# Kernel optimization log

Hardware: AMD Instinct MI355X
Metric: run time of the kernel (lower is better)

The kernel has to match this reference:

```python
import jax, jax.numpy as jnp
import numpy as np

# ---- static module configuration ----
N_POU = 16
N_BC = 3
P = N_POU + N_BC          # full_n_pou = 19
F = 3                      # n_fields
B, N, D_IN, D_Z, D_H = 16, 1024, 32, 64, 64
N_DIR = 64
MAX_ITERS = 50
ALPHA = 0.1                # damped fixed-point step of the nonlinear solver

# edge_pairs / delta_0 for the complete graph on P POU nodes (construct_delta0)
_ei, _ej = np.triu_indices(P, 1)
E = _ei.shape[0]           # n_one_forms = P*(P-1)/2 = 171
_d0 = np.zeros((E, P), np.float32)
_d0[np.arange(E), _ei] = -1.0
_d0[np.arange(E), _ej] = 1.0
DELTA0 = jnp.asarray(_d0)  # [E, P]
EI = jnp.asarray(_ei)
EJ = jnp.asarray(_ej)


def setup_inputs() -> dict:
    key = jax.random.key(0)
    ks = jax.random.split(key, 16)
    f32 = jnp.float32
    inp = {
        'in_tokens': jax.random.normal(ks[0], (B, N, D_IN), f32),
        'K_list': 0.02 * jax.random.normal(ks[1], (B, F, N, N), f32),
        'M_list': 0.02 * jax.random.normal(ks[2], (B, F, N, N), f32),
        'dirichlet_nodes': jax.random.randint(ks[3], (B, N_DIR), 0, N),
        'boundary_vals': jax.random.normal(ks[4], (B, N_DIR, F), f32),
        'u_init': jax.random.normal(ks[5], (B, P * F), f32),
        # learned parameters (encoder / source_model / boundary_w / flux_model)
        'W_enc': jax.random.normal(ks[6], (D_IN, D_Z), f32) / np.sqrt(D_IN),
        'b_enc': jnp.zeros((D_Z,), f32),
        'W_src': jax.random.normal(ks[7], (D_Z, F), f32) / np.sqrt(D_Z),
        'b_src': jnp.zeros((F,), f32),
        'W_pou': jax.random.normal(ks[8], (D_Z, P * F), f32) / np.sqrt(D_Z),
        'Wf1': jax.random.normal(ks[9], (2 * F, D_H), f32) / np.sqrt(2 * F),
        'Wz': jax.random.normal(ks[10], (D_Z, D_H), f32) / np.sqrt(D_Z),
        'bf': jnp.zeros((D_H,), f32),
        'Wf2': 0.1 * jax.random.normal(ks[11], (D_H, F), f32) / np.sqrt(D_H),
    }
    return inp


def reference(in_tokens, K_list, M_list, dirichlet_nodes, boundary_vals, u_init,
              W_enc, b_enc, W_src, b_src, W_pou, Wf1, Wz, bf, Wf2):
    Bc, Nn = in_tokens.shape[0], in_tokens.shape[1]
    latent_scaling = Nn / P

    # encoder: in_tokens -> per-node latents z [B,N,Dz]
    z = jnp.tanh(in_tokens @ W_enc + b_enc)

    # boundary_w: partition-of-unity weights W [B,P,N,F], boundary POUs biased
    # toward Dirichlet nodes via boundary_vals
    logits = (z @ W_pou).reshape(Bc, Nn, P, F)
    bidx = jnp.arange(Bc)[:, None]
    bvals_full = jnp.zeros((Bc, Nn, F), in_tokens.dtype).at[bidx, dirichlet_nodes].set(boundary_vals)
    logits = logits.at[:, :, P - N_BC:, :].add(bvals_full[:, :, None, :])
    Wmat = jax.nn.softmax(logits, axis=2).transpose(0, 2, 1, 3)  # [B,P,N,F]

    # source_model + latent projection (source_mode='identity' -> pass-through)
    f_full = z @ W_src + b_src                                    # [B,N,F]
    f_latent = jnp.einsum('bpif,bif->bpf', Wmat, f_full) / latent_scaling

    # project_bilinear_per_field: K_hat[b,p,q,f] = W K W^T / scaling
    def project(Kl):
        t = jnp.einsum('bpif,bfij->bpjf', Wmat, Kl)               # [B,P,N,F]
        return jnp.einsum('bpjf,bqjf->bpqf', t, Wmat) / latent_scaling

    # apply_dirichlet_per_field: boundary rows -> identity
    eyeP = jnp.eye(P, dtype=in_tokens.dtype)
    row_mask = jnp.zeros((P,), bool).at[P - N_BC:].set(True)
    def dirichlet_bilinear(Kh):
        return jnp.where(row_mask[None, :, None, None], eyeP[None, :, :, None], Kh)

    K_hat = dirichlet_bilinear(project(K_list))                   # [B,P,P,F]
    M_hat = dirichlet_bilinear(project(M_list))

    bc_mask = jnp.zeros((P, F), bool).at[P - N_BC:, :].set(True)
    bc_vals = jnp.zeros((P, F), in_tokens.dtype).at[P - N_BC, :].set(1.0)

    # flux_model conditioning: pooled latent, precomputed once
    zp = jnp.mean(z, axis=1) @ Wz                                 # [B,Dh]
    src_term = jnp.einsum('bpqf,bqf->bpf', M_hat, f_latent)       # constant in u

    def G(u_flat):  # G_residual
        u = u_flat.reshape(Bc, P, F)
        diff_term = jnp.einsum('bpqf,bqf->bpf', K_hat, u)
        ue = jnp.concatenate([u[:, EI], u[:, EJ]], axis=-1)       # [B,E,2F]
        flux = jnp.tanh(ue @ Wf1 + zp[:, None, :] + bf) @ Wf2     # [B,E,F]
        flux_term = jnp.einsum('ep,bef->bpf', DELTA0, flux)
        r = diff_term - src_term - flux_term
        r = jnp.where(bc_mask[None], u - bc_vals[None], r)        # Dirichlet residual
        return r.reshape(Bc, -1)

    # NonlinearSolver: damped fixed-point iteration, fixed MAX_ITERS under jit
    def step(u, _):
        return u - ALPHA * G(u), None
    u_hat, _ = jax.lax.scan(step, u_init, None, length=MAX_ITERS)

    u_coarse = u_hat.reshape(Bc, P, F)
    u_fine = jnp.einsum('bpif,bpf->bif', Wmat, u_coarse)          # [B,N,F]
    return u_fine
```

## Files before the change

kernel.cpp:

```cpp
#include <hip/hip_runtime.h>

#define Bn 16
#define Nn 1024
#define DIN 32
#define DZ 64
#define Fc 3
#define Pp 19
#define PPAD 20
#define Ee 171
#define ITERS 50
#define INV_SCALE (19.0f/1024.0f)
#define CHUNK 64
#define PF 4

#define OFF_WPROJ 0
#define OFF_FFULL 983040
#define OFF_FLAT  1033216
#define OFF_UBUF  1034128
#define OFF_BVALS 1035040
#define OFF_ZACC  1084192
#define OFF_KHAT  1085216
#define OFF_SRC   1099808
#define ZERO_FLOATS 65536

__global__ __launch_bounds__(1024) void k_scatter(const int* __restrict__ nodes,
                                                  const float* __restrict__ bvals,
                                                  float* __restrict__ bfull) {
  __shared__ int sn[1024];
  int tid = threadIdx.x;
  sn[tid] = nodes[tid];
  __syncthreads();
  int b = tid >> 6, j = tid & 63;
  int node = sn[tid];
  bool win = true;
  for (int j2 = j + 1; j2 < 64; j2++)
    if (sn[(b << 6) | j2] == node) { win = false; break; }
  if (win) {
    #pragma unroll
    for (int f = 0; f < Fc; f++)
      bfull[((size_t)b*Nn + node)*Fc + f] = bvals[(size_t)tid*Fc + f];
  }
}

__global__ __launch_bounds__(128) void k_encode(
    const float* __restrict__ x, const float* __restrict__ Wenc, const float* __restrict__ benc,
    const float* __restrict__ Wsrc, const float* __restrict__ bsrc, const float* __restrict__ Wpou,
    const float* __restrict__ bfull, float* __restrict__ wproj, float* __restrict__ ffull,
    float* __restrict__ zacc) {
  __shared__ float sWenc[DIN*DZ];
  __shared__ float sWpou[DZ*57];
  __shared__ float sWsrc[DZ*Fc];
  int tid = threadIdx.x;
  for (int t = tid; t < DIN*DZ; t += 128) sWenc[t] = Wenc[t];
  for (int t = tid; t < DZ*57; t += 128) sWpou[t] = Wpou[t];
  for (int t = tid; t < DZ*Fc; t += 128) sWsrc[t] = Wsrc[t];
  __syncthreads();
  int g = blockIdx.x*128 + tid;
  int b = g >> 10, i = g & 1023;
  float xr[DIN];
  const float* xp = x + (size_t)g*DIN;
  #pragma unroll
  for (int k = 0; k < DIN; k += 4) {
    float4 t4 = *(const float4*)(xp + k);
    xr[k] = t4.x; xr[k+1] = t4.y; xr[k+2] = t4.z; xr[k+3] = t4.w;
  }
  float l[57];
  #pragma unroll
  for (int o = 0; o < 57; o++) l[o] = 0.f;
  float ff[3] = {bsrc[0], bsrc[1], bsrc[2]};
  int lane = tid & 63;
  for (int d = 0; d < DZ; d++) {
    float zd = benc[d];
    #pragma unroll
    for (int k = 0; k < DIN; k++) zd = fmaf(xr[k], sWenc[k*DZ + d], zd);
    zd = tanhf(zd);
    #pragma unroll
    for (int o = 0; o < 57; o++) l[o] = fmaf(zd, sWpou[d*57 + o], l[o]);
    #pragma unroll
    for (int f = 0; f < Fc; f++) ff[f] = fmaf(zd, sWsrc[d*Fc + f], ff[f]);
    float zs = zd;
    #pragma unroll
    for (int off = 32; off > 0; off >>= 1) zs += __shfl_xor(zs, off, 64);
    if (lane == 0) atomicAdd(&zacc[b*DZ + d], zs);
  }
  #pragma unroll
  for (int f = 0; f < Fc; f++) ffull[(size_t)g*Fc + f] = ff[f];
  #pragma unroll
  for (int f = 0; f < Fc; f++) {
    float bv = bfull[(size_t)g*Fc + f];
    l[16*3+f] += bv; l[17*3+f] += bv; l[18*3+f] += bv;
  }
  #pragma unroll
  for (int f = 0; f < Fc; f++) {
    float m = l[f];
    #pragma unroll
    for (int p = 1; p < Pp; p++) m = fmaxf(m, l[p*3+f]);
    float ex[Pp]; float s = 0.f;
    #pragma unroll
    for (int p = 0; p < Pp; p++) { ex[p] = __expf(l[p*3+f] - m); s += ex[p]; }
    float inv = 1.f / s;
    float* wp = wproj + ((size_t)(b*Fc + f)*Nn + i)*PPAD;
    #pragma unroll
    for (int p = 0; p < Pp; p++) wp[p] = ex[p]*inv;
  }
}

__global__ __launch_bounds__(256) void k_flat(const float* __restrict__ wproj,
                                              const float* __restrict__ ffull,
                                              float* __restrict__ flat) {
  int bf = blockIdx.x;
  int b = bf / 3, f = bf % 3;
  float acc[Pp];
  #pragma unroll
  for (int q = 0; q < Pp; q++) acc[q] = 0.f;
  for (int i = threadIdx.x; i < Nn; i += 256) {
    float fv = ffull[((size_t)b*Nn + i)*Fc + f];
    const float* row = wproj + ((size_t)bf*Nn + i)*PPAD;
    #pragma unroll
    for (int q = 0; q < Pp; q++) acc[q] = fmaf(row[q], fv, acc[q]);
  }
  #pragma unroll
  for (int q = 0; q < Pp; q++) {
    float v = acc[q];
    #pragma unroll
    for (int off = 32; off > 0; off >>= 1) v += __shfl_xor(v, off, 64);
    acc[q] = v;
  }
  __shared__ float red[4][Pp];
  int wave = threadIdx.x >> 6, lane = threadIdx.x & 63;
  if (lane == 0) {
    #pragma unroll
    for (int q = 0; q < Pp; q++) red[wave][q] = acc[q];
  }
  __syncthreads();
  if (threadIdx.x < Pp) {
    float s = red[0][threadIdx.x] + red[1][threadIdx.x] + red[2][threadIdx.x] + red[3][threadIdx.x];
    flat[bf*Pp + threadIdx.x] = s * INV_SCALE;
  }
}

__global__ __launch_bounds__(256, 1) void k_project(
    const float* __restrict__ Kl, const float* __restrict__ Ml,
    const float* __restrict__ wproj, const float* __restrict__ flat,
    float* __restrict__ khat, float* __restrict__ srca) {
  __shared__ float sW[16*CHUNK];
  int chunk = blockIdx.x;
  int bf = blockIdx.y;
  int i0 = chunk * CHUNK;
  const float* Kb = Kl + (size_t)bf*Nn*Nn + (size_t)i0*Nn;
  const float* Mb = Ml + (size_t)bf*Nn*Nn + (size_t)i0*Nn;
  const float* Wp = wproj + (size_t)bf*Nn*PPAD;
  const float* Wrow0 = Wp + (size_t)i0*PPAD;
  int tid = threadIdx.x;

  for (int t = tid; t < 16*CHUNK; t += 256) {
    int r = t >> 4, p = t & 15;
    sW[p*CHUNK + r] = Wrow0[r*PPAD + p];
  }

  float fl[Pp];
  #pragma unroll
  for (int q = 0; q < Pp; q++) fl[q] = flat[bf*Pp + q];
  int j0 = tid * 4;
  float v[4];
  #pragma unroll
  for (int r = 0; r < 4; r++) {
    const float* row = Wp + (size_t)(j0 + r)*PPAD;
    float s = 0.f;
    #pragma unroll
    for (int q = 0; q < Pp; q++) s = fmaf(row[q], fl[q], s);
    v[r] = s;
  }
  __syncthreads();

  float4 acc[16];
  float sa[16];
  #pragma unroll
  for (int p = 0; p < 16; p++) {
    acc[p].x = 0.f; acc[p].y = 0.f; acc[p].z = 0.f; acc[p].w = 0.f;
    sa[p] = 0.f;
  }

  const float* kp = Kb + j0;
  const float* mp = Mb + j0;
  float4 kbuf[PF], mbuf[PF];
  #pragma unroll
  for (int s = 0; s < PF; s++) {
    kbuf[s] = *(const float4*)(kp + (size_t)s*Nn);
    mbuf[s] = *(const float4*)(mp + (size_t)s*Nn);
  }
  for (int ii = 0; ii < CHUNK; ii += PF) {
    #pragma unroll
    for (int s = 0; s < PF; s++) {
      float4 k4 = kbuf[s], m4 = mbuf[s];
      int nxt = (ii + PF + s) & (CHUNK - 1);
      kbuf[s] = *(const float4*)(kp + (size_t)nxt*Nn);
      mbuf[s] = *(const float4*)(mp + (size_t)nxt*Nn);
      float tm = m4.x*v[0] + m4.y*v[1] + m4.z*v[2] + m4.w*v[3];
      const float* wrow = &sW[ii + s];
      #pragma unroll
      for (int p = 0; p < 16; p++) {
        float wv = wrow[p*CHUNK];
        acc[p].x = fmaf(wv, k4.x, acc[p].x);
        acc[p].y = fmaf(wv, k4.y, acc[p].y);
        acc[p].z = fmaf(wv, k4.z, acc[p].z);
        acc[p].w = fmaf(wv, k4.w, acc[p].w);
        sa[p] = fmaf(wv, tm, sa[p]);
      }
    }
  }

  int lane = tid & 63;
  #pragma unroll
  for (int q = 0; q < Pp; q++) {
    float w0 = Wp[(size_t)(j0 + 0)*PPAD + q];
    float w1 = Wp[(size_t)(j0 + 1)*PPAD + q];
    float w2 = Wp[(size_t)(j0 + 2)*PPAD + q];
    float w3 = Wp[(size_t)(j0 + 3)*PPAD + q];
    float pr[16];
    #pragma unroll
    for (int p = 0; p < 16; p++)
      pr[p] = acc[p].x*w0 + acc[p].y*w1 + acc[p].z*w2 + acc[p].w*w3;
    #pragma unroll
    for (int p = 0; p < 16; p++) {
      float vq = pr[p];
      #pragma unroll
      for (int off = 32; off > 0; off >>= 1) vq += __shfl_xor(vq, off, 64);
      pr[p] = vq;
    }
    if (lane == 0) {
      #pragma unroll
      for (int p = 0; p < 16; p++)
        atomicAdd(&khat[(bf*16 + p)*Pp + q], pr[p] * INV_SCALE);
    }
  }
  #pragma unroll
  for (int p = 0; p < 16; p++) {
    float vq = sa[p];
    #pragma unroll
    for (int off = 32; off > 0; off >>= 1) vq += __shfl_xor(vq, off, 64);
    sa[p] = vq;
  }
  if (lane == 0) {
    #pragma unroll
    for (int p = 0; p < 16; p++) atomicAdd(&srca[bf*16 + p], sa[p] * INV_SCALE);
  }
}

#define ABS 65
__global__ __launch_bounds__(704, 1) void k_solve(
    const float* __restrict__ khat, const float* __restrict__ srca,
    const float* __restrict__ zacc, const float* __restrict__ Wz,
    const float* __restrict__ u_init, const float* __restrict__ Wf1,
    const float* __restrict__ bfv, const float* __restrict__ Wf2,
    float* __restrict__ ubuf) {
  int b = blockIdx.x;
  __shared__ float u_s[57];
  __shared__ float flux_s[Ee*Fc];
  __shared__ float sW1[6*DZ];
  __shared__ float sW2[DZ*Fc];
  __shared__ float sbz[DZ];
  __shared__ float sK[Fc*16*Pp];
  __shared__ float ssrc[Fc*16];
  __shared__ float sA[Pp*ABS];
  __shared__ float sB[Pp*ABS];
  int tid = threadIdx.x;
  for (int t = tid; t < 6*DZ; t += 704) sW1[t] = Wf1[t];
  for (int t = tid; t < DZ*Fc; t += 704) sW2[t] = Wf2[t];
  if (tid < DZ) {
    float s = 0.f;
    for (int k = 0; k < DZ; k++) s = fmaf(zacc[b*DZ + k], Wz[k*DZ + tid], s);
    sbz[tid] = bfv[tid] + s * (1.f/1024.f);
  }
  for (int t = tid; t < Fc*16*Pp; t += 704) sK[t] = khat[b*Fc*16*Pp + t];
  if (tid < 48) ssrc[tid] = srca[b*48 + tid];
  if (tid < 57) u_s[tid] = u_init[b*57 + tid];
  __syncthreads();
  int e = tid >> 2, h = tid & 3;
  bool active = (tid < 4*Ee);
  int ei = 0, ej = 0;
  if (active) {
    int r = e, i = 0;
    while (r >= 18 - i) { r -= 18 - i; i++; }
    ei = i; ej = i + 1 + r;
  }
  int d0 = h * 16;
  for (int it = 0; it < ITERS; it++) {
    for (int t = tid; t < 2*Pp*DZ; t += 704) {
      int half = (t >= Pp*DZ);
      int t2 = half ? t - Pp*DZ : t;
      int p = t2 >> 6, d = t2 & 63;
      const float* w1 = sW1 + (half ? 3*DZ : 0) + d;
      float s = u_s[p*3+0]*w1[0] + u_s[p*3+1]*w1[DZ] + u_s[p*3+2]*w1[2*DZ];
      (half ? sB : sA)[p*ABS + d] = s;
    }
    __syncthreads();
    if (active) {
      const float* Ap = sA + ei*ABS;
      const float* Bp = sB + ej*ABS;
      float fl0 = 0.f, fl1 = 0.f, fl2 = 0.f;
      for (int dd = 0; dd < 16; dd++) {
        int d = d0 + dd;
        float pre = sbz[d] + Ap[d] + Bp[d];
        float xc = fminf(fmaxf(pre, -20.f), 20.f);
        float t = __expf(2.f * xc);
        float th = (t - 1.f) / (t + 1.f);
        fl0 = fmaf(th, sW2[d*3 + 0], fl0);
        fl1 = fmaf(th, sW2[d*3 + 1], fl1);
        fl2 = fmaf(th, sW2[d*3 + 2], fl2);
      }
      fl0 += __shfl_xor(fl0, 1, 64); fl0 += __shfl_xor(fl0, 2, 64);
      fl1 += __shfl_xor(fl1, 1, 64); fl1 += __shfl_xor(fl1, 2, 64);
      fl2 += __shfl_xor(fl2, 1, 64); fl2 += __shfl_xor(fl2, 2, 64);
      if (h == 0) { flux_s[e*3+0] = fl0; flux_s[e*3+1] = fl1; flux_s[e*3+2] = fl2; }
    }
    __syncthreads();
    if (tid < 57) {
      int p = tid / 3, f = tid % 3;
      float u_old = u_s[tid];
      float r_;
      if (p < 16) {
        float diff = 0.f;
        for (int q = 0; q < Pp; q++) diff = fmaf(sK[(f*16 + p)*Pp + q], u_s[q*3 + f], diff);
        float ft = 0.f;
        for (int o = 0; o < Pp; o++) {
          if (o == p) continue;
          int i_ = (o < p) ? o : p;
          int j_ = (o < p) ? p : o;
          int eidx = i_*Pp - (i_*(i_+1))/2 + (j_ - i_ - 1);
          float sgn = (o < p) ? 1.f : -1.f;
          ft += sgn * flux_s[eidx*3 + f];
        }
        r_ = diff - ssrc[f*16 + p] - ft;
      } else {
        r_ = u_old - ((p == 16) ? 1.f : 0.f);
      }
      u_s[tid] = u_old - 0.1f * r_;
    }
    __syncthreads();
  }
  if (tid < 57) ubuf[b*57 + tid] = u_s[tid];
}

__global__ __launch_bounds__(256) void k_out(const float* __restrict__ wproj,
                                             const float* __restrict__ ubuf,
                                             float* __restrict__ out) {
  __shared__ float u_s[57];
  int b = blockIdx.y;
  int i = blockIdx.x*256 + threadIdx.x;
  if (threadIdx.x < 57) u_s[threadIdx.x] = ubuf[b*57 + threadIdx.x];
  __syncthreads();
  #pragma unroll
  for (int f = 0; f < Fc; f++) {
    const float* row = wproj + ((size_t)(b*Fc + f)*Nn + i)*PPAD;
    float s = 0.f;
    #pragma unroll
    for (int p = 0; p < Pp; p++) s = fmaf(row[p], u_s[p*3 + f], s);
    out[((size_t)b*Nn + i)*Fc + f] = s;
  }
}

extern "C" void kernel_launch(void* const* d_in, const int* in_sizes, int n_in,
                              void* d_out, int out_size, void* d_ws, size_t ws_size,
                              hipStream_t stream) {
  const float* in_tokens = (const float*)d_in[0];
  const float* K_list    = (const float*)d_in[1];
  const float* M_list    = (const float*)d_in[2];
  const int*   dnodes    = (const int*)d_in[3];
  const float* bvals     = (const float*)d_in[4];
  const float* u_init    = (const float*)d_in[5];
  const float* W_enc     = (const float*)d_in[6];
  const float* b_enc     = (const float*)d_in[7];
  const float* W_src     = (const float*)d_in[8];
  const float* b_src     = (const float*)d_in[9];
  const float* W_pou     = (const float*)d_in[10];
  const float* Wf1       = (const float*)d_in[11];
  const float* Wz        = (const float*)d_in[12];
  const float* bfv       = (const float*)d_in[13];
  const float* Wf2       = (const float*)d_in[14];
  float* ws  = (float*)d_ws;
  float* out = (float*)d_out;

  float* WPROJ = ws + OFF_WPROJ;
  float* FFULL = ws + OFF_FFULL;
  float* FLAT  = ws + OFF_FLAT;
  float* UBUF  = ws + OFF_UBUF;
  float* BVALS = ws + OFF_BVALS;
  float* ZACC  = ws + OFF_ZACC;
  float* KHAT  = ws + OFF_KHAT;
  float* SRC   = ws + OFF_SRC;

  hipMemsetAsync(ws + OFF_BVALS, 0, (size_t)ZERO_FLOATS * sizeof(float), stream);
  k_scatter<<<1, 1024, 0, stream>>>(dnodes, bvals, BVALS);
  k_encode<<<128, 128, 0, stream>>>(in_tokens, W_enc, b_enc, W_src, b_src, W_pou,
                                    BVALS, WPROJ, FFULL, ZACC);
  k_flat<<<Bn*Fc, 256, 0, stream>>>(WPROJ, FFULL, FLAT);
  k_project<<<dim3(Nn/CHUNK, Bn*Fc), 256, 0, stream>>>(K_list, M_list, WPROJ, FLAT, KHAT, SRC);
  k_solve<<<Bn, 704, 0, stream>>>(KHAT, SRC, ZACC, Wz, u_init, Wf1, bfv, Wf2, UBUF);
  k_out<<<dim3(Nn/256, Bn), 256, 0, stream>>>(WPROJ, UBUF, out);
}
```

Before: 863.7 us.

## Split K/M projection passes and defer W-contraction to a separate reduction kernel

The fused K/M projection kernel is split into two sequential streaming passes. It no longer contracts with W in its epilogue. Instead it writes per-chunk partial products to a large workspace buffer, and a new k_khat kernel sums them and applies the W projection with atomics. Launch bounds go from 1 to 4 blocks per SM to raise occupancy for the bandwidth-bound stream over K and M, and the shared-memory W load index order is changed. This costs an extra ~50MB workspace write and read plus one more launch, and it falls back to the old kernel when the workspace is too small.

```diff
diff --git a/kernel.cpp b/kernel.cpp
--- a/kernel.cpp
+++ b/kernel.cpp
@@ -22,6 +22,8 @@
 #define OFF_KHAT  1085216
 #define OFF_SRC   1099808
 #define ZERO_FLOATS 65536
+#define OFF_TPART 1100576
+#define NEED_FLOATS (OFF_TPART + 48*16*16*1024)
 
 __global__ __launch_bounds__(1024) void k_scatter(const int* __restrict__ nodes,
                                                   const float* __restrict__ bvals,
@@ -139,7 +141,144 @@
   }
 }
 
-__global__ __launch_bounds__(256, 1) void k_project(
+__global__ __launch_bounds__(256, 4) void k_project(
+    const float* __restrict__ Kl, const float* __restrict__ Ml,
+    const float* __restrict__ wproj, const float* __restrict__ flat,
+    float* __restrict__ tpart, float* __restrict__ srca) {
+  __shared__ float sW[16*CHUNK];
+  int chunk = blockIdx.x;
+  int bf = blockIdx.y;
+  int i0 = chunk * CHUNK;
+  const float* Kb = Kl + (size_t)bf*Nn*Nn + (size_t)i0*Nn;
+  const float* Mb = Ml + (size_t)bf*Nn*Nn + (size_t)i0*Nn;
+  const float* Wp = wproj + (size_t)bf*Nn*PPAD;
+  const float* Wrow0 = Wp + (size_t)i0*PPAD;
+  int tid = threadIdx.x;
+
+  for (int t = tid; t < 16*CHUNK; t += 256) {
+    int r = t & (CHUNK-1), p = t >> 6;
+    sW[p*CHUNK + r] = Wrow0[r*PPAD + p];
+  }
+
+  float fl[Pp];
+  #pragma unroll
+  for (int q = 0; q < Pp; q++) fl[q] = flat[bf*Pp + q];
+  int j0 = tid * 4;
+  float v0, v1, v2, v3;
+  {
+    float vv[4];
+    #pragma unroll
+    for (int r = 0; r < 4; r++) {
+      const float* row = Wp + (size_t)(j0 + r)*PPAD;
+      float s = 0.f;
+      #pragma unroll
+      for (int q = 0; q < Pp; q++) s = fmaf(row[q], fl[q], s);
+      vv[r] = s;
+    }
+    v0 = vv[0]; v1 = vv[1]; v2 = vv[2]; v3 = vv[3];
+  }
+  __syncthreads();
+
+  float4 acc[16];
+  #pragma unroll
+  for (int p = 0; p < 16; p++) { acc[p].x = 0.f; acc[p].y = 0.f; acc[p].z = 0.f; acc[p].w = 0.f; }
+  {
+    const float* kp = Kb + j0;
+    float4 kbuf[PF];
+    #pragma unroll
+    for (int s = 0; s < PF; s++) kbuf[s] = *(const float4*)(kp + (size_t)s*Nn);
+    for (int ii = 0; ii < CHUNK; ii += PF) {
+      #pragma unroll
+      for (int s = 0; s < PF; s++) {
+        float4 k4 = kbuf[s];
+        int nxt = (ii + PF + s) & (CHUNK - 1);
+        kbuf[s] = *(const float4*)(kp + (size_t)nxt*Nn);
+        const float* wrow = &sW[ii + s];
+        #pragma unroll
+        for (int p = 0; p < 16; p++) {
+          float wv = wrow[p*CHUNK];
+          acc[p].x = fmaf(wv, k4.x, acc[p].x);
+          acc[p].y = fmaf(wv, k4.y, acc[p].y);
+          acc[p].z = fmaf(wv, k4.z, acc[p].z);
+          acc[p].w = fmaf(wv, k4.w, acc[p].w);
+        }
+      }
+    }
+  }
+  {
+    float* tp = tpart + ((size_t)(bf*16 + chunk)*16)*Nn + j0;
+    #pragma unroll
+    for (int p = 0; p < 16; p++) *(float4*)(tp + (size_t)p*Nn) = acc[p];
+  }
+
+  float sa[16];
+  #pragma unroll
+  for (int p = 0; p < 16; p++) sa[p] = 0.f;
+  {
+    const float* mp = Mb + j0;
+    float4 mbuf[PF];
+    #pragma unroll
+    for (int s = 0; s < PF; s++) mbuf[s] = *(const float4*)(mp + (size_t)s*Nn);
+    for (int ii = 0; ii < CHUNK; ii += PF) {
+      #pragma unroll
+      for (int s = 0; s < PF; s++) {
+        float4 m4 = mbuf[s];
+        int nxt = (ii + PF + s) & (CHUNK - 1);
+        mbuf[s] = *(const float4*)(mp + (size_t)nxt*Nn);
+        float tm = m4.x*v0 + m4.y*v1 + m4.z*v2 + m4.w*v3;
+        const float* wrow = &sW[ii + s];
+        #pragma unroll
+        for (int p = 0; p < 16; p++) sa[p] = fmaf(wrow[p*CHUNK], tm, sa[p]);
+      }
+    }
+  }
+  int lane = tid & 63;
+  #pragma unroll
+  for (int p = 0; p < 16; p++) {
+    float vq = sa[p];
+    #pragma unroll
+    for (int off = 32; off > 0; off >>= 1) vq += __shfl_xor(vq, off, 64);
+    sa[p] = vq;
+  }
+  if (lane == 0) {
+    #pragma unroll
+    for (int p = 0; p < 16; p++) atomicAdd(&srca[bf*16 + p], sa[p] * INV_SCALE);
+  }
+}
+
+__global__ __launch_bounds__(256) void k_khat(const float* __restrict__ tpart,
+                                              const float* __restrict__ wproj,
+                                              float* __restrict__ khat) {
+  __shared__ float sT[16*64];
+  __shared__ float sWq[64*PPAD];
+  int jb = blockIdx.x, bf = blockIdx.y;
+  int tid = threadIdx.x;
+  {
+    int id = tid * 4;
+    int p = id >> 6;
+    int r = id & 63;
+    const float* base = tpart + ((size_t)(bf*16)*16 + p)*Nn + jb*64 + r;
+    float4 s4 = make_float4(0.f, 0.f, 0.f, 0.f);
+    #pragma unroll 4
+    for (int c = 0; c < 16; c++) {
+      float4 t4 = *(const float4*)(base + (size_t)c*16*Nn);
+      s4.x += t4.x; s4.y += t4.y; s4.z += t4.z; s4.w += t4.w;
+    }
+    *(float4*)&sT[p*64 + r] = s4;
+  }
+  const float* wsrc = wproj + ((size_t)bf*Nn + jb*64)*PPAD;
+  for (int t = tid; t < 64*PPAD; t += 256) sWq[t] = wsrc[t];
+  __syncthreads();
+  for (int o = tid; o < 16*Pp; o += 256) {
+    int p = o / Pp, q = o - p*Pp;
+    float s = 0.f;
+    #pragma unroll
+    for (int r = 0; r < 64; r++) s = fmaf(sT[p*64 + r], sWq[r*PPAD + q], s);
+    atomicAdd(&khat[(bf*16 + p)*Pp + q], s * INV_SCALE);
+  }
+}
+
+__global__ __launch_bounds__(256, 1) void k_project_fb(
     const float* __restrict__ Kl, const float* __restrict__ Ml,
     const float* __restrict__ wproj, const float* __restrict__ flat,
     float* __restrict__ khat, float* __restrict__ srca) {
@@ -152,12 +291,10 @@
   const float* Wp = wproj + (size_t)bf*Nn*PPAD;
   const float* Wrow0 = Wp + (size_t)i0*PPAD;
   int tid = threadIdx.x;
-
   for (int t = tid; t < 16*CHUNK; t += 256) {
-    int r = t >> 4, p = t & 15;
+    int r = t & (CHUNK-1), p = t >> 6;
     sW[p*CHUNK + r] = Wrow0[r*PPAD + p];
   }
-
   float fl[Pp];
   #pragma unroll
   for (int q = 0; q < Pp; q++) fl[q] = flat[bf*Pp + q];
@@ -172,7 +309,6 @@
     v[r] = s;
   }
   __syncthreads();
-
   float4 acc[16];
   float sa[16];
   #pragma unroll
@@ -180,7 +316,6 @@
     acc[p].x = 0.f; acc[p].y = 0.f; acc[p].z = 0.f; acc[p].w = 0.f;
     sa[p] = 0.f;
   }
-
   const float* kp = Kb + j0;
   const float* mp = Mb + j0;
   float4 kbuf[PF], mbuf[PF];
@@ -209,7 +344,6 @@
       }
     }
   }
-
   int lane = tid & 63;
   #pragma unroll
   for (int q = 0; q < Pp; q++) {
@@ -389,13 +523,19 @@
   float* ZACC  = ws + OFF_ZACC;
   float* KHAT  = ws + OFF_KHAT;
   float* SRC   = ws + OFF_SRC;
+  float* TPART = ws + OFF_TPART;
 
   hipMemsetAsync(ws + OFF_BVALS, 0, (size_t)ZERO_FLOATS * sizeof(float), stream);
   k_scatter<<<1, 1024, 0, stream>>>(dnodes, bvals, BVALS);
   k_encode<<<128, 128, 0, stream>>>(in_tokens, W_enc, b_enc, W_src, b_src, W_pou,
                                     BVALS, WPROJ, FFULL, ZACC);
   k_flat<<<Bn*Fc, 256, 0, stream>>>(WPROJ, FFULL, FLAT);
-  k_project<<<dim3(Nn/CHUNK, Bn*Fc), 256, 0, stream>>>(K_list, M_list, WPROJ, FLAT, KHAT, SRC);
+  if (ws_size >= (size_t)NEED_FLOATS * sizeof(float)) {
+    k_project<<<dim3(Nn/CHUNK, Bn*Fc), 256, 0, stream>>>(K_list, M_list, WPROJ, FLAT, TPART, SRC);
+    k_khat<<<dim3(16, Bn*Fc), 256, 0, stream>>>(TPART, WPROJ, KHAT);
+  } else {
+    k_project_fb<<<dim3(Nn/CHUNK, Bn*Fc), 256, 0, stream>>>(K_list, M_list, WPROJ, FLAT, KHAT, SRC);
+  }
   k_solve<<<Bn, 704, 0, stream>>>(KHAT, SRC, ZACC, Wz, u_init, Wf1, bfv, Wf2, UBUF);
   k_out<<<dim3(Nn/256, Bn), 256, 0, stream>>>(WPROJ, UBUF, out);
 }
```

Result: faster. 791.6 us (-8.3%).
